# Performance work log

Measured on AMD Instinct MI355X. Metric: run time of the kernel, lower is better.

The kernel has to match this reference:

```python
import jax, jax.numpy as jnp
import numpy as np

LN_EPS = 1e-5


def layer_norm(x, g, b):
    m = jnp.mean(x, axis=-1, keepdims=True)
    v = jnp.mean(jnp.square(x - m), axis=-1, keepdims=True)
    return (x - m) * jax.lax.rsqrt(v + LN_EPS) * g + b


def sym_norm(A):
    # D^{-1/2} (A + I) D^{-1/2}
    N = A.shape[0]
    Ah = A + jnp.eye(N, dtype=A.dtype)
    d = jnp.sum(Ah, axis=-1)
    dinv = jax.lax.rsqrt(jnp.maximum(d, 1e-12))
    return Ah * dinv[:, None] * dinv[None, :]


def gru_layer(xs, Wih, Whh, bih, bhh):
    # xs: (BN, T, Din) -> ys: (BN, T, H). PyTorch GRU cell math.
    BN, T, _ = xs.shape
    H = Whh.shape[1]
    x_proj = xs @ Wih.T + bih  # (BN, T, 3H), precompute input projections

    def step(h, xp):
        hp = h @ Whh.T + bhh
        xr, xz, xn = jnp.split(xp, 3, axis=-1)
        hr, hz, hn = jnp.split(hp, 3, axis=-1)
        r = jax.nn.sigmoid(xr + hr)
        z = jax.nn.sigmoid(xz + hz)
        n = jnp.tanh(xn + r * hn)
        h_new = (1.0 - z) * n + z * h
        return h_new, h_new

    h0 = jnp.zeros((BN, H), xs.dtype)
    _, ys = jax.lax.scan(step, h0, jnp.swapaxes(x_proj, 0, 1))
    return jnp.swapaxes(ys, 0, 1)


def amscf_forward(x, A, FSP, DSP,
                  E1, E2, fus_W, fus_b, fus_v, beta1, beta2,
                  gcn_W1, gcn_b1, ln1_g, ln1_b, gcn_W2, gcn_b2, ln2_g, ln2_b,
                  gru_Wih0, gru_Whh0, gru_bih0, gru_bhh0,
                  gru_Wih1, gru_Whh1, gru_bih1, gru_bhh1,
                  att_w, fc1_W, fc1_b, fc2_W, fc2_b):
    B, T, N, _ = x.shape
    Hor = fc2_W.shape[0]

    # ImprovedAdjacency: blend A with adaptive node-embedding adjacency
    Aadp = jax.nn.softmax(jax.nn.relu(E1 @ E2.T), axis=-1)
    IA = 0.5 * A + 0.5 * Aadp

    # fuse_with_A with learned gates
    w1 = jax.nn.sigmoid(beta1)
    w2 = jax.nn.sigmoid(beta2)
    C1 = w1 * A + (1.0 - w1) * FSP
    C2 = w2 * A + (1.0 - w2) * DSP

    # TransposeAttentionFusion: graph-level attention over the 3 candidate graphs
    Gs = jnp.stack([IA, C1, C2], axis=0)  # (3, N, N)
    sc = jnp.mean(jnp.tanh(Gs @ fus_W.T + fus_b) @ fus_v, axis=-1)  # (3,)
    alpha = jax.nn.softmax(sc)
    MG = jnp.einsum('k,knm->nm', alpha, Gs)

    S_hat = sym_norm(MG)  # (N, N)

    # TwoLayerGCN over all (B, T) at once: act(LN(S X W1)) -> LN(S h W2)
    xf = x.reshape(B * T, N, 1)
    h = jnp.einsum('mn,bnc->bmc', S_hat, xf) @ gcn_W1 + gcn_b1
    h = jax.nn.relu(layer_norm(h, ln1_g, ln1_b))
    g = jnp.einsum('mn,bnc->bmc', S_hat, h) @ gcn_W2 + gcn_b2
    g = layer_norm(g, ln2_g, ln2_b)  # (B*T, N, C)

    C = g.shape[-1]
    # Faithful to original: raw view of (B, T, N, C) into (B*N, T, C)
    H_seq = g.reshape(B, T, N, C).reshape(B * N, T, C)

    out = gru_layer(H_seq, gru_Wih0, gru_Whh0, gru_bih0, gru_bhh0)
    out = gru_layer(out, gru_Wih1, gru_Whh1, gru_bih1, gru_bhh1)  # (BN, T, Hg)

    # SoftAttentionPooling over time
    score = out @ att_w  # (BN, T)
    att = jax.nn.softmax(score, axis=1)
    ctx = jnp.einsum('bt,bth->bh', att, out)

    hfc = jax.nn.gelu(ctx @ fc1_W.T + fc1_b)
    dlt = hfc @ fc2_W.T + fc2_b  # (BN, Hor); dropout is identity at eval
    return jnp.transpose(dlt.reshape(B, N, Hor), (0, 2, 1))  # (B, Hor, N)


def setup_inputs() -> dict:
    B, T, N, Hor = 32, 12, 1000, 12
    Cin, Ch, Cout, Hg, Da, De = 1, 96, 96, 192, 32, 10
    key = jax.random.key(0)
    ks = jax.random.split(key, 32)
    f32 = jnp.float32

    def nrm(k, shape, scale):
        return jax.random.normal(k, shape, dtype=f32) * scale

    inp = {
        'x': jax.random.normal(ks[0], (B, T, N, Cin), dtype=f32),
        'A': jax.random.uniform(ks[1], (N, N), dtype=f32),
        'FSP': jax.random.uniform(ks[2], (N, N), dtype=f32),
        'DSP': jax.random.uniform(ks[3], (N, N), dtype=f32),
        'E1': nrm(ks[4], (N, De), 0.1),
        'E2': nrm(ks[5], (N, De), 0.1),
        'fus_W': nrm(ks[6], (Da, N), 1.0 / np.sqrt(N)),
        'fus_b': jnp.zeros((Da,), f32),
        'fus_v': nrm(ks[7], (Da,), 1.0 / np.sqrt(Da)),
        'beta1': jnp.float32(0.5),
        'beta2': jnp.float32(0.5),
        'gcn_W1': nrm(ks[8], (Cin, Ch), 1.0 / np.sqrt(Cin)),
        'gcn_b1': jnp.zeros((Ch,), f32),
        'ln1_g': jnp.ones((Ch,), f32),
        'ln1_b': jnp.zeros((Ch,), f32),
        'gcn_W2': nrm(ks[9], (Ch, Cout), 1.0 / np.sqrt(Ch)),
        'gcn_b2': jnp.zeros((Cout,), f32),
        'ln2_g': jnp.ones((Cout,), f32),
        'ln2_b': jnp.zeros((Cout,), f32),
        'gru_Wih0': nrm(ks[10], (3 * Hg, Cout), 1.0 / np.sqrt(Hg)),
        'gru_Whh0': nrm(ks[11], (3 * Hg, Hg), 1.0 / np.sqrt(Hg)),
        'gru_bih0': jnp.zeros((3 * Hg,), f32),
        'gru_bhh0': jnp.zeros((3 * Hg,), f32),
        'gru_Wih1': nrm(ks[12], (3 * Hg, Hg), 1.0 / np.sqrt(Hg)),
        'gru_Whh1': nrm(ks[13], (3 * Hg, Hg), 1.0 / np.sqrt(Hg)),
        'gru_bih1': jnp.zeros((3 * Hg,), f32),
        'gru_bhh1': jnp.zeros((3 * Hg,), f32),
        'att_w': nrm(ks[14], (Hg,), 1.0 / np.sqrt(Hg)),
        'fc1_W': nrm(ks[15], (Hg, Hg), 1.0 / np.sqrt(Hg)),
        'fc1_b': jnp.zeros((Hg,), f32),
        'fc2_W': nrm(ks[16], (Hor, Hg), 1.0 / np.sqrt(Hg)),
        'fc2_b': jnp.zeros((Hor,), f32),
    }
    return inp


def reference(x, A, FSP, DSP, E1, E2, fus_W, fus_b, fus_v, beta1, beta2,
              gcn_W1, gcn_b1, ln1_g, ln1_b, gcn_W2, gcn_b2, ln2_g, ln2_b,
              gru_Wih0, gru_Whh0, gru_bih0, gru_bhh0,
              gru_Wih1, gru_Whh1, gru_bih1, gru_bhh1,
              att_w, fc1_W, fc1_b, fc2_W, fc2_b):
    return amscf_forward(x, A, FSP, DSP, E1, E2, fus_W, fus_b, fus_v, beta1, beta2,
                         gcn_W1, gcn_b1, ln1_g, ln1_b, gcn_W2, gcn_b2, ln2_g, ln2_b,
                         gru_Wih0, gru_Whh0, gru_bih0, gru_bhh0,
                         gru_Wih1, gru_Whh1, gru_bih1, gru_bhh1,
                         att_w, fc1_W, fc1_b, fc2_W, fc2_b)
```

## Files before the change

### kernel.cpp

```cpp
#include <hip/hip_runtime.h>

typedef unsigned short u16;
typedef unsigned int u32;
typedef __attribute__((ext_vector_type(8))) short short8;
typedef __attribute__((ext_vector_type(4))) float float4v;

#define DEV static __device__ __forceinline__

DEV float bf2f(u16 u) { u32 x = ((u32)u) << 16; float f; __builtin_memcpy(&f, &x, 4); return f; }
DEV u16 f2bf(float f) {
  u32 u; __builtin_memcpy(&u, &f, 4);
  u = (u + 0x7fffu + ((u >> 16) & 1u)) >> 16;
  return (u16)u;
}
DEV float sigm(float x) { return 1.f / (1.f + __expf(-x)); }

DEV void gl16(const u16* g, u16* l) {
  __builtin_amdgcn_global_load_lds(
      (const __attribute__((address_space(1))) void*)g,
      (__attribute__((address_space(3))) void*)l, 16, 0, 0);
}

template <int OMODE>
__launch_bounds__(256)
__global__ void gemm_nt(const u16* __restrict__ A, int lda,
                        const u16* __restrict__ B, int ldb,
                        void* __restrict__ Cp, int ldc,
                        int M, int N, int K,
                        const float* __restrict__ bias)
{
  constexpr int PK = 40;
  __shared__ u16 As[128 * PK];
  __shared__ u16 Bs[64 * PK];

  const int tid  = threadIdx.x;
  const int m0   = blockIdx.y * 128;
  const int n0   = blockIdx.x * 64;
  const int wid  = tid >> 6;
  const int lane = tid & 63;
  const int l15  = lane & 15;
  const int quad = lane >> 4;
  const int wm   = (wid >> 1) * 64;
  const int wn   = (wid & 1) * 32;

  float4v acc[4][2];
  const float4v fz = {0.f, 0.f, 0.f, 0.f};
#pragma unroll
  for (int i = 0; i < 4; i++)
#pragma unroll
    for (int j = 0; j < 2; j++) acc[i][j] = fz;

  const int arow = tid >> 2;
  const int akc  = tid & 3;

  const int kt_count = (K + 31) / 32;
  for (int kt = 0; kt < kt_count; ++kt) {
    const int k0 = kt * 32 + akc * 8;
    const bool kok = (k0 < K);
    uint4 av0 = make_uint4(0, 0, 0, 0), av1 = av0, bv = av0;
    int ra = m0 + arow;
    if (kok && ra < M)        av0 = *(const uint4*)(A + (size_t)ra * lda + k0);
    if (kok && ra + 64 < M)   av1 = *(const uint4*)(A + (size_t)(ra + 64) * lda + k0);
    int rb = n0 + arow;
    if (kok && rb < N)        bv  = *(const uint4*)(B + (size_t)rb * ldb + k0);

    __syncthreads();
    *(uint4*)&As[arow * PK + akc * 8]        = av0;
    *(uint4*)&As[(arow + 64) * PK + akc * 8] = av1;
    *(uint4*)&Bs[arow * PK + akc * 8]        = bv;
    __syncthreads();

    short8 af[4], bfr[2];
#pragma unroll
    for (int i = 0; i < 4; i++)
      af[i] = *(const short8*)&As[(wm + i * 16 + l15) * PK + quad * 8];
#pragma unroll
    for (int j = 0; j < 2; j++)
      bfr[j] = *(const short8*)&Bs[(wn + j * 16 + l15) * PK + quad * 8];
#pragma unroll
    for (int i = 0; i < 4; i++)
#pragma unroll
      for (int j = 0; j < 2; j++)
        acc[i][j] = __builtin_amdgcn_mfma_f32_16x16x32_bf16(af[i], bfr[j], acc[i][j], 0, 0, 0);
  }

#pragma unroll
  for (int i = 0; i < 4; i++)
#pragma unroll
    for (int j = 0; j < 2; j++)
#pragma unroll
      for (int e = 0; e < 4; e++) {
        int r = m0 + wm + i * 16 + quad * 4 + e;
        int c = n0 + wn + j * 16 + l15;
        if (r < M && c < N) {
          float v = acc[i][j][e];
          if (OMODE == 0) ((float*)Cp)[(size_t)r * ldc + c] = v;
          else {
            float a = v + bias[c];
            float t = tanhf(0.7978845608028654f * (a + 0.044715f * a * a * a));
            ((float*)Cp)[(size_t)r * ldc + c] = 0.5f * a * (1.f + t);
          }
        }
      }
}

__launch_bounds__(256)
__global__ void k_bigemm(const u16* __restrict__ A,
                         const u16* __restrict__ B,
                         const float* __restrict__ b2, const float* __restrict__ g2,
                         const float* __restrict__ be2,
                         u16* __restrict__ Gg)
{
  __shared__ u16 As[128 * 64];
  __shared__ u16 Bs[96 * 64];
  __shared__ float stats[2][2][128];

  const int tid  = threadIdx.x;
  const int bid  = blockIdx.x;
  const int xcd  = bid & 7;
  const int jj   = bid >> 3;
  const int m0   = (jj & 7) * 128;
  const int rt   = xcd + 8 * (jj >> 3);

  const int wid  = tid >> 6;
  const int lane = tid & 63;
  const int l15  = lane & 15;
  const int quad = lane >> 4;
  const int wm   = (wid >> 1) * 64;
  const int wn   = (wid & 1) * 48;
  const int wni  = wid & 1;

  const int srow8 = lane >> 3;
  const int sw8   = ((lane & 7) ^ srow8) * 8;

  const u16* abase = A + (size_t)(m0 + wid * 8 + srow8) * 1024 + sw8;
  const u16* bbase = B + (size_t)(rt * 96 + wid * 8 + srow8) * 1024 + sw8;

  float4v acc[4][3];
  const float4v fz = {0.f, 0.f, 0.f, 0.f};
#pragma unroll
  for (int i = 0; i < 4; i++)
#pragma unroll
    for (int j = 0; j < 3; j++) acc[i][j] = fz;

  for (int kt = 0; kt < 16; ++kt) {
    const int ko = kt * 64;
#pragma unroll
    for (int c = 0; c < 4; c++)
      gl16(abase + (size_t)c * 32 * 1024 + ko, &As[(c * 32 + wid * 8) * 64]);
#pragma unroll
    for (int c = 0; c < 3; c++)
      gl16(bbase + (size_t)c * 32 * 1024 + ko, &Bs[(c * 32 + wid * 8) * 64]);
    __syncthreads();
#pragma unroll
    for (int k32 = 0; k32 < 2; k32++) {
      const int swr = ((quad + 4 * k32) ^ (l15 & 7)) * 8;
      short8 af[4], bf[3];
#pragma unroll
      for (int i = 0; i < 4; i++)
        af[i] = *(const short8*)&As[(wm + i * 16 + l15) * 64 + swr];
#pragma unroll
      for (int j = 0; j < 3; j++)
        bf[j] = *(const short8*)&Bs[(wn + j * 16 + l15) * 64 + swr];
#pragma unroll
      for (int i = 0; i < 4; i++)
#pragma unroll
        for (int j = 0; j < 3; j++)
          acc[i][j] = __builtin_amdgcn_mfma_f32_16x16x32_bf16(af[i], bf[j], acc[i][j], 0, 0, 0);
    }
    __syncthreads();
  }

  float b2v[3], g2v[3], bev[3];
#pragma unroll
  for (int j = 0; j < 3; j++) {
    int c = wn + j * 16 + l15;
    b2v[j] = b2[c]; g2v[j] = g2[c]; bev[j] = be2[c];
  }
#pragma unroll
  for (int i = 0; i < 4; i++)
#pragma unroll
    for (int e = 0; e < 4; e++) {
      float s = 0.f, ss = 0.f;
#pragma unroll
      for (int j = 0; j < 3; j++) {
        float v = acc[i][j][e] + b2v[j];
        acc[i][j][e] = v;
        s += v; ss += v * v;
      }
      s += __shfl_xor(s, 1); ss += __shfl_xor(ss, 1);
      s += __shfl_xor(s, 2); ss += __shfl_xor(ss, 2);
      s += __shfl_xor(s, 4); ss += __shfl_xor(ss, 4);
      s += __shfl_xor(s, 8); ss += __shfl_xor(ss, 8);
      if (l15 == 0) {
        int rl = wm + i * 16 + quad * 4 + e;
        stats[wni][0][rl] = s;
        stats[wni][1][rl] = ss;
      }
    }
  __syncthreads();
#pragma unroll
  for (int i = 0; i < 4; i++)
#pragma unroll
    for (int e = 0; e < 4; e++) {
      int rl = wm + i * 16 + quad * 4 + e;
      int m = m0 + rl;
      if (m < 1000) {
        float ts  = stats[0][0][rl] + stats[1][0][rl];
        float tss = stats[0][1][rl] + stats[1][1][rl];
        float mean = ts * (1.f / 96.f);
        float var  = tss * (1.f / 96.f) - mean * mean;
        float isd  = rsqrtf(var + 1e-5f);
#pragma unroll
        for (int j = 0; j < 3; j++) {
          int c = wn + j * 16 + l15;
          Gg[(size_t)rt * 96000 + (size_t)m * 96 + c] =
              f2bf((acc[i][j][e] - mean) * isd * g2v[j] + bev[j]);
        }
      }
    }
}

DEV void pool_fold(int m0, int c0, int pm,
                   const u16* __restrict__ Hpool,
                   const float* __restrict__ score_rd,
                   const float* __restrict__ Mrd, const float* __restrict__ Lrd,
                   float* __restrict__ Mwr, float* __restrict__ Lwr,
                   float* __restrict__ Nvp)
{
  const int tid = threadIdx.x;
#pragma unroll
  for (int k = 0; k < 16; k++) {
    int idx = k * 256 + tid;
    int ql = idx >> 5, cl = idx & 31;
    int q = m0 + ql, c = c0 + cl;
    size_t nidx = (size_t)q * 192 + c;
    float s = score_rd[q];
    float hnew = bf2f(Hpool[nidx]);
    float so, wnf, prev;
    if (pm == 1) { so = 0.f; wnf = 1.f; prev = 0.f; }
    else {
      float Mo = Mrd[q];
      float Mn = fmaxf(Mo, s);
      so = __expf(Mo - Mn); wnf = __expf(s - Mn);
      prev = Nvp[nidx];
    }
    Nvp[nidx] = prev * so + wnf * hnew;
  }
  if (c0 == 0 && tid < 128) {
    int q = m0 + tid;
    float s = score_rd[q];
    if (pm == 1) { Mwr[q] = s; Lwr[q] = 1.f; }
    else {
      float Mo = Mrd[q], Mn = fmaxf(Mo, s);
      Mwr[q] = Mn;
      Lwr[q] = Lrd[q] * __expf(Mo - Mn) + __expf(s - Mn);
    }
  }
}

template <int KX, bool POOL>
DEV void gru_tile(u16* As, u16* Bs,
                  int m0, int c0,
                  const u16* __restrict__ Xin, int ldx,
                  const u16* __restrict__ Win,
                  const u16* __restrict__ Hin,
                  const u16* __restrict__ Whh,
                  const float* __restrict__ bih, const float* __restrict__ bhh,
                  u16* __restrict__ Hout,
                  const float* __restrict__ att_w,
                  float* __restrict__ score_acc,
                  const u16* __restrict__ Hpool,
                  const float* __restrict__ score_rd,
                  const float* __restrict__ Mrd, const float* __restrict__ Lrd,
                  float* __restrict__ Mwr, float* __restrict__ Lwr,
                  float* __restrict__ Nvp,
                  int t0, int pm)
{
  const int tid  = threadIdx.x;
  const int wid  = tid >> 6;
  const int lane = tid & 63;
  const int l15  = lane & 15;
  const int quad = lane >> 4;
  const int wm   = wid * 32;

  if (!POOL && pm)
    pool_fold(m0, c0, pm, Hpool, score_rd, Mrd, Lrd, Mwr, Lwr, Nvp);

  const int srow8 = lane >> 3;
  const int sw8   = ((lane & 7) ^ srow8) * 8;
  const int srow4 = lane >> 2;
  const int sw4   = ((lane & 3) ^ ((lane >> 3) & 3)) * 8;

  float4v aR[2][2], aZ[2][2], aXN[2][2], aHN[2][2];
  const float4v fz = {0.f, 0.f, 0.f, 0.f};
#pragma unroll
  for (int i = 0; i < 2; i++)
#pragma unroll
    for (int j = 0; j < 2; j++) { aR[i][j] = fz; aZ[i][j] = fz; aXN[i][j] = fz; aHN[i][j] = fz; }

  if (KX == 96) {
    const u16* ax0 = Xin + (size_t)(m0 + wid * 16 + srow4) * ldx + sw4;
    const u16* ax1 = Xin + (size_t)(m0 + 64 + wid * 16 + srow4) * ldx + sw4;
    const int b0 = wid * 16 + srow4;
    const u16* bx0 = Win + (size_t)((b0 >> 5) * 192 + c0 + (b0 & 31)) * 96 + sw4;
    const int b1 = 64 + wid * 16 + srow4;
    const u16* bx1 = Win + (size_t)(384 + c0 + (b1 & 31)) * 96 + sw4;
    u16* asl0 = &As[(wid * 16) * 32];
    u16* asl1 = &As[(64 + wid * 16) * 32];
    u16* bsl0 = &Bs[(wid * 16) * 32];
    u16* bsl1 = &Bs[(64 + wid * 16) * 32];
    const int swa = (quad ^ ((l15 >> 1) & 3)) * 8;
#pragma unroll
    for (int kt = 0; kt < 3; ++kt) {
      const int ko = kt * 32;
      gl16(ax0 + ko, asl0); gl16(ax1 + ko, asl1);
      gl16(bx0 + ko, bsl0);
      if (wid < 2) gl16(bx1 + ko, bsl1);
      __syncthreads();
      short8 af[2], bR[2], bZ[2], bN[2];
#pragma unroll
      for (int i = 0; i < 2; i++)
        af[i] = *(const short8*)&As[(wm + i * 16 + l15) * 32 + swa];
#pragma unroll
      for (int j = 0; j < 2; j++) {
        bR[j] = *(const short8*)&Bs[(j * 16 + l15) * 32 + swa];
        bZ[j] = *(const short8*)&Bs[(32 + j * 16 + l15) * 32 + swa];
        bN[j] = *(const short8*)&Bs[(64 + j * 16 + l15) * 32 + swa];
      }
#pragma unroll
      for (int i = 0; i < 2; i++)
#pragma unroll
        for (int j = 0; j < 2; j++) {
          aR[i][j]  = __builtin_amdgcn_mfma_f32_16x16x32_bf16(af[i], bR[j], aR[i][j], 0, 0, 0);
          aZ[i][j]  = __builtin_amdgcn_mfma_f32_16x16x32_bf16(af[i], bZ[j], aZ[i][j], 0, 0, 0);
          aXN[i][j] = __builtin_amdgcn_mfma_f32_16x16x32_bf16(af[i], bN[j], aXN[i][j], 0, 0, 0);
        }
      __syncthreads();
    }
  } else {
    const u16* abase = Xin + (size_t)(m0 + wid * 8 + srow8) * 192 + sw8;
    const u16* bbase = Win + (size_t)(c0 + wid * 8 + srow8) * 192 + sw8;
#pragma unroll
    for (int kt = 0; kt < 3; ++kt) {
      const int ko = kt * 64;
#pragma unroll
      for (int c = 0; c < 4; c++)
        gl16(abase + (size_t)c * 32 * 192 + ko, &As[(c * 32 + wid * 8) * 64]);
#pragma unroll
      for (int c = 0; c < 3; c++)
        gl16(bbase + (size_t)c * 192 * 192 + ko, &Bs[(c * 32 + wid * 8) * 64]);
      __syncthreads();
#pragma unroll
      for (int k32 = 0; k32 < 2; k32++) {
        const int swr = ((quad + 4 * k32) ^ (l15 & 7)) * 8;
        short8 af[2], bR[2], bZ[2], bN[2];
#pragma unroll
        for (int i = 0; i < 2; i++)
          af[i] = *(const short8*)&As[(wm + i * 16 + l15) * 64 + swr];
#pragma unroll
        for (int j = 0; j < 2; j++) {
          bR[j] = *(const short8*)&Bs[(j * 16 + l15) * 64 + swr];
          bZ[j] = *(const short8*)&Bs[(32 + j * 16 + l15) * 64 + swr];
          bN[j] = *(const short8*)&Bs[(64 + j * 16 + l15) * 64 + swr];
        }
#pragma unroll
        for (int i = 0; i < 2; i++)
#pragma unroll
          for (int j = 0; j < 2; j++) {
            aR[i][j]  = __builtin_amdgcn_mfma_f32_16x16x32_bf16(af[i], bR[j], aR[i][j], 0, 0, 0);
            aZ[i][j]  = __builtin_amdgcn_mfma_f32_16x16x32_bf16(af[i], bZ[j], aZ[i][j], 0, 0, 0);
            aXN[i][j] = __builtin_amdgcn_mfma_f32_16x16x32_bf16(af[i], bN[j], aXN[i][j], 0, 0, 0);
          }
      }
      __syncthreads();
    }
  }
  if (!t0) {
    const u16* abase = Hin + (size_t)(m0 + wid * 8 + srow8) * 192 + sw8;
    const u16* bbase = Whh + (size_t)(c0 + wid * 8 + srow8) * 192 + sw8;
#pragma unroll
    for (int kt = 0; kt < 3; ++kt) {
      const int ko = kt * 64;
#pragma unroll
      for (int c = 0; c < 4; c++)
        gl16(abase + (size_t)c * 32 * 192 + ko, &As[(c * 32 + wid * 8) * 64]);
#pragma unroll
      for (int c = 0; c < 3; c++)
        gl16(bbase + (size_t)c * 192 * 192 + ko, &Bs[(c * 32 + wid * 8) * 64]);
      __syncthreads();
#pragma unroll
      for (int k32 = 0; k32 < 2; k32++) {
        const int swr = ((quad + 4 * k32) ^ (l15 & 7)) * 8;
        short8 af[2], bR[2], bZ[2], bN[2];
#pragma unroll
        for (int i = 0; i < 2; i++)
          af[i] = *(const short8*)&As[(wm + i * 16 + l15) * 64 + swr];
#pragma unroll
        for (int j = 0; j < 2; j++) {
          bR[j] = *(const short8*)&Bs[(j * 16 + l15) * 64 + swr];
          bZ[j] = *(const short8*)&Bs[(32 + j * 16 + l15) * 64 + swr];
          bN[j] = *(const short8*)&Bs[(64 + j * 16 + l15) * 64 + swr];
        }
#pragma unroll
        for (int i = 0; i < 2; i++)
#pragma unroll
          for (int j = 0; j < 2; j++) {
            aR[i][j]  = __builtin_amdgcn_mfma_f32_16x16x32_bf16(af[i], bR[j], aR[i][j], 0, 0, 0);
            aZ[i][j]  = __builtin_amdgcn_mfma_f32_16x16x32_bf16(af[i], bZ[j], aZ[i][j], 0, 0, 0);
            aHN[i][j] = __builtin_amdgcn_mfma_f32_16x16x32_bf16(af[i], bN[j], aHN[i][j], 0, 0, 0);
          }
      }
      __syncthreads();
    }
  }

  float ps[2][4];
  if (POOL) {
#pragma unroll
    for (int i = 0; i < 2; i++)
#pragma unroll
      for (int e = 0; e < 4; e++) ps[i][e] = 0.f;
  }
#pragma unroll
  for (int j = 0; j < 2; ++j) {
    const int c = c0 + j * 16 + l15;
    const float brz = bih[c] + bhh[c];
    const float bzz = bih[192 + c] + bhh[192 + c];
    const float bxn = bih[384 + c];
    const float bhn = bhh[384 + c];
    const float aw  = POOL ? att_w[c] : 0.f;
#pragma unroll
    for (int i = 0; i < 2; ++i)
#pragma unroll
      for (int e = 0; e < 4; ++e) {
        const int row = m0 + wm + i * 16 + quad * 4 + e;
        float rg  = sigm(aR[i][j][e] + brz);
        float zg  = sigm(aZ[i][j][e] + bzz);
        float hnv = bhn + (t0 ? 0.f : aHN[i][j][e]);
        float ng  = tanhf(aXN[i][j][e] + bxn + rg * hnv);
        float hold = t0 ? 0.f : bf2f(Hin[(size_t)row * 192 + c]);
        float hnew = (1.f - zg) * ng + zg * hold;
        Hout[(size_t)row * 192 + c] = f2bf(hnew);
        if (POOL) ps[i][e] += hnew * aw;
      }
  }
  if (POOL) {
#pragma unroll
    for (int i = 0; i < 2; ++i)
#pragma unroll
      for (int e = 0; e < 4; ++e) {
        float v = ps[i][e];
        v += __shfl_xor(v, 1); v += __shfl_xor(v, 2);
        v += __shfl_xor(v, 4); v += __shfl_xor(v, 8);
        if (l15 == 0) atomicAdd(&score_acc[m0 + wm + i * 16 + quad * 4 + e], v);
      }
  }
}

struct GruArgs {
  const u16 *Gg, *Wih0, *Whh0, *Wih1, *Whh1;
  const float *bih0, *bhh0, *bih1, *bhh1, *att_w;
  u16 *h0[2];
  u16 *h1[3];
  float *M[2], *L[2], *s[3];
  float* Nv;
};

__launch_bounds__(256)
__global__ void k_gru2(GruArgs a, int u)
{
  __shared__ u16 As[128 * 64];
  __shared__ u16 Bs[96 * 64];
  const int m0 = blockIdx.y * 128;

  if (blockIdx.x < 6) {
    const int c0 = blockIdx.x * 32;
    const int pm = (u < 2) ? 0 : (u == 2 ? 1 : 2);
    if (u > 11) {
      if (pm)
        pool_fold(m0, c0, pm, a.h1[(u + 1) % 3], a.s[(u + 1) % 3],
                  a.M[(u + 1) & 1], a.L[(u + 1) & 1], a.M[u & 1], a.L[u & 1], a.Nv);
      return;
    }
    if (c0 == 0 && threadIdx.x < 128) a.s[u % 3][m0 + threadIdx.x] = 0.f;
    gru_tile<96, false>(As, Bs, m0, c0,
        a.Gg + u * 96, 1152, a.Wih0, a.h0[u & 1], a.Whh0, a.bih0, a.bhh0, a.h0[(u & 1) ^ 1],
        nullptr, nullptr,
        a.h1[(u + 1) % 3], a.s[(u + 1) % 3],
        a.M[(u + 1) & 1], a.L[(u + 1) & 1],
        a.M[u & 1], a.L[u & 1],
        a.Nv, u == 0, pm);
  } else {
    if (u < 1) return;
    const int t = u - 1;
    const int c0 = (blockIdx.x - 6) * 32;
    gru_tile<192, true>(As, Bs, m0, c0,
        a.h0[u & 1], 192, a.Wih1, a.h1[(u + 1) % 3], a.Whh1, a.bih1, a.bhh1, a.h1[t % 3],
        a.att_w, a.s[t % 3],
        nullptr, nullptr, nullptr, nullptr, nullptr, nullptr, nullptr,
        t == 0, 0);
  }
}

__launch_bounds__(256)
__global__ void k_pool(const u16* __restrict__ H, const float* __restrict__ score_rd,
                       const float* __restrict__ Mrd, const float* __restrict__ Lrd,
                       float* __restrict__ Lwr, float* __restrict__ Nv)
{
  const int base = blockIdx.x * 1536;
  const int tid  = threadIdx.x;
#pragma unroll
  for (int k = 0; k < 6; k++) {
    const int idx = base + tid + k * 256;
    const int q = idx / 192;
    const float s = score_rd[q];
    const float Mo = Mrd[q];
    const float Mn = fmaxf(Mo, s);
    const float so = __expf(Mo - Mn);
    const float wn = __expf(s - Mn);
    Nv[idx] = Nv[idx] * so + wn * bf2f(H[idx]);
  }
  if (tid < 8) {
    const int q = blockIdx.x * 8 + tid;
    const float s = score_rd[q];
    const float Mo = Mrd[q];
    const float Mn = fmaxf(Mo, s);
    Lwr[q] = Lrd[q] * __expf(Mo - Mn) + __expf(s - Mn);
  }
}

__launch_bounds__(256)
__global__ void k_h2gemm(const float* __restrict__ yt, const float4* __restrict__ cwpk,
                         const u16* __restrict__ W2s, const float* __restrict__ consts,
                         u16* __restrict__ h2t)
{
  constexpr int PK = 40;
  __shared__ u16 As[128 * PK];
  __shared__ u16 Bs[96 * PK];
  __shared__ u16 Ts[96 * 136];

  const int tid  = threadIdx.x;
  const int m0   = blockIdx.x * 128;
  const int wid  = tid >> 6;
  const int lane = tid & 63;
  const int l15  = lane & 15;
  const int quad = lane >> 4;
  const int wm   = (wid >> 1) * 64;
  const int wn   = (wid & 1) * 48;

  const float P = consts[0], Q = consts[1], VW = consts[2], CWB = consts[3], VB = consts[4];

  const int arow = tid >> 2;
  const int akc  = tid & 3;

  float yv[2], mu[2], iv[2];
#pragma unroll
  for (int rr = 0; rr < 2; rr++) {
    int i = m0 + arow + rr * 64;
    int r = i / 1000, n = i - r * 1000;
    float y = yt[n * 384 + r];
    yv[rr] = y;
    mu[rr] = y * P + Q;
    iv[rr] = rsqrtf(y * y * VW + 2.f * y * CWB + VB + 1e-5f);
  }

  float4v acc[4][3];
  const float4v fz = {0.f, 0.f, 0.f, 0.f};
#pragma unroll
  for (int i = 0; i < 4; i++)
#pragma unroll
    for (int j = 0; j < 3; j++) acc[i][j] = fz;

  uint4 asave[2][3];
  const bool has2 = (arow < 32);

  for (int kt = 0; kt < 6; ++kt) {
    const int k0 = kt * 32 + akc * 8;
    uint4 av[2];
    if (kt < 3) {
#pragma unroll
      for (int rr = 0; rr < 2; rr++) {
        u16 hb[8];
#pragma unroll
        for (int e = 0; e < 8; e++) {
          float4 cw = cwpk[k0 + e];
          float t = yv[rr] * cw.x + cw.y - mu[rr];
          float h = fmaxf(t * iv[rr] * cw.z + cw.w, 0.f);
          hb[e] = f2bf(h);
        }
        __builtin_memcpy(&av[rr], hb, 16);
        asave[rr][kt] = av[rr];
      }
    } else {
      av[0] = asave[0][kt - 3];
      av[1] = asave[1][kt - 3];
    }
    uint4 bv0 = *(const uint4*)(W2s + (size_t)arow * 192 + k0);
    uint4 bv1 = make_uint4(0, 0, 0, 0);
    if (has2) bv1 = *(const uint4*)(W2s + (size_t)(arow + 64) * 192 + k0);

    __syncthreads();
    *(uint4*)&As[arow * PK + akc * 8]        = av[0];
    *(uint4*)&As[(arow + 64) * PK + akc * 8] = av[1];
    *(uint4*)&Bs[arow * PK + akc * 8]        = bv0;
    if (has2) *(uint4*)&Bs[(arow + 64) * PK + akc * 8] = bv1;
    __syncthreads();

    short8 af[4], bfr[3];
#pragma unroll
    for (int i = 0; i < 4; i++)
      af[i] = *(const short8*)&As[(wm + i * 16 + l15) * PK + quad * 8];
#pragma unroll
    for (int j = 0; j < 3; j++)
      bfr[j] = *(const short8*)&Bs[(wn + j * 16 + l15) * PK + quad * 8];
#pragma unroll
    for (int i = 0; i < 4; i++)
#pragma unroll
      for (int j = 0; j < 3; j++)
        acc[i][j] = __builtin_amdgcn_mfma_f32_16x16x32_bf16(af[i], bfr[j], acc[i][j], 0, 0, 0);
  }

#pragma unroll
  for (int i = 0; i < 4; i++)
#pragma unroll
    for (int j = 0; j < 3; j++)
#pragma unroll
      for (int e = 0; e < 4; e++) {
        int rowl = wm + i * 16 + quad * 4 + e;
        int c2   = wn + j * 16 + l15;
        Ts[c2 * 136 + rowl] = f2bf(acc[i][j][e]);
      }
  __syncthreads();
#pragma unroll
  for (int u = tid; u < 1536; u += 256) {
    int c2 = u >> 4, ch = u & 15;
    int iidx0 = m0 + ch * 8;
    int r = iidx0 / 1000, n0 = iidx0 - r * 1000;
    *(uint4*)(h2t + (size_t)(r * 96 + c2) * 1024 + n0) = *(const uint4*)&Ts[c2 * 136 + ch * 8];
  }
}

__launch_bounds__(256)
__global__ void k_prep(const float* x, const float* fus_W,
                       const float* Wih0, const float* Whh0,
                       const float* Wih1, const float* Whh1,
                       const float* gcn_W1, const float* gcn_b1,
                       const float* gcn_W2, const float* ln1g, const float* ln1b,
                       u16* xbf, u16* fusWbf, u16* Wih0b, u16* Whh0b, u16* Wih1b, u16* Whh1b,
                       u16* W2s, float4* cwpk, float* consts)
{
  long o = (long)blockIdx.x * 256 + threadIdx.x;
  if (o < 384000) xbf[o] = f2bf(x[o]);
  else if ((o -= 384000) < 32000) fusWbf[o] = f2bf(fus_W[o]);
  else if ((o -= 32000) < 55296)  Wih0b[o] = f2bf(Wih0[o]);
  else if ((o -= 55296) < 110592) Whh0b[o] = f2bf(Whh0[o]);
  else if ((o -= 110592) < 110592) Wih1b[o] = f2bf(Wih1[o]);
  else if ((o -= 110592) < 110592) Whh1b[o] = f2bf(Whh1[o]);
  else if ((o -= 110592) < 9216) {
    int c2 = (int)o / 96, c = (int)o - c2 * 96;
    float wv = gcn_W2[c * 96 + c2];
    u16 hi = f2bf(wv);
    u16 lo = f2bf(wv - bf2f(hi));
    W2s[c2 * 192 + c] = hi;
    W2s[c2 * 192 + 96 + c] = lo;
  }
  else if ((o -= 9216) < 96) {
    int c = (int)o;
    float4 cw;
    cw.x = gcn_W1[c]; cw.y = gcn_b1[c]; cw.z = ln1g[c]; cw.w = ln1b[c];
    cwpk[c] = cw;
  }
  if (blockIdx.x == 0 && threadIdx.x == 0) {
    float sw = 0, sb = 0, sww = 0, swb = 0, sbb = 0;
    for (int c = 0; c < 96; c++) {
      float wv = gcn_W1[c], b = gcn_b1[c];
      sw += wv; sb += b; sww += wv * wv; swb += wv * b; sbb += b * b;
    }
    float P = sw / 96.f, Q = sb / 96.f;
    consts[0] = P; consts[1] = Q;
    consts[2] = sww / 96.f - P * P;
    consts[3] = swb / 96.f - P * Q;
    consts[4] = sbb / 96.f - Q * Q;
  }
}

__launch_bounds__(256)
__global__ void k_zero(u16* __restrict__ h2t, float* __restrict__ s0,
                       float* __restrict__ s1, float* __restrict__ s2)
{
  int idx = blockIdx.x * 256 + threadIdx.x;
  if (idx < 110592) {
    int row = idx / 3, p = idx - row * 3;
    *(uint4*)(h2t + (size_t)row * 1024 + 1000 + p * 8) = make_uint4(0, 0, 0, 0);
  } else if ((idx -= 110592) < 32000) {
    s0[idx] = 0.f;
  } else if ((idx -= 32000) < 32000) {
    s1[idx] = 0.f;
  } else if ((idx -= 32000) < 32000) {
    s2[idx] = 0.f;
  }
}

__launch_bounds__(256)
__global__ void k_w1split(const float* __restrict__ fc1W, u16* __restrict__ w1s)
{
  int idx = blockIdx.x * 256 + threadIdx.x;
  if (idx >= 192 * 192) return;
  int n = idx / 192, k = idx - n * 192;
  float w = fc1W[idx];
  u16 hi = f2bf(w);
  u16 lo = f2bf(w - bf2f(hi));
  w1s[(size_t)n * 576 + k]       = hi;
  w1s[(size_t)n * 576 + 192 + k] = lo;
  w1s[(size_t)n * 576 + 384 + k] = hi;
}

__launch_bounds__(256)
__global__ void k_adjrow(const float* __restrict__ A, const float* __restrict__ FSP,
                         const float* __restrict__ DSP, const float* __restrict__ E1,
                         const float* __restrict__ E2,
                         const float* beta1, const float* beta2,
                         u16* __restrict__ G, float* __restrict__ rowsums)
{
  __shared__ float z[1000];
  __shared__ float red[256];
  const int n = blockIdx.x, tid = threadIdx.x;

  float e1r[10];
#pragma unroll
  for (int d = 0; d < 10; d++) e1r[d] = E1[n * 10 + d];

  float lmax = -1e30f;
  for (int m = tid; m < 1000; m += 256) {
    float s = 0;
#pragma unroll
    for (int d = 0; d < 10; d++) s += e1r[d] * E2[m * 10 + d];
    s = fmaxf(s, 0.f);
    z[m] = s;
    lmax = fmaxf(lmax, s);
  }
  red[tid] = lmax; __syncthreads();
  for (int st = 128; st > 0; st >>= 1) { if (tid < st) red[tid] = fmaxf(red[tid], red[tid + st]); __syncthreads(); }
  const float mx = red[0]; __syncthreads();

  float lsum = 0;
  for (int m = tid; m < 1000; m += 256) { float e = __expf(z[m] - mx); z[m] = e; lsum += e; }
  red[tid] = lsum; __syncthreads();
  for (int st = 128; st > 0; st >>= 1) { if (tid < st) red[tid] += red[tid + st]; __syncthreads(); }
  const float inv = 1.f / red[0]; __syncthreads();

  const float w1 = sigm(beta1[0]);
  const float w2 = sigm(beta2[0]);
  float s0 = 0, s1 = 0, s2 = 0;
  for (int m = tid; m < 1000; m += 256) {
    float aadp = z[m] * inv;
    float a = A[n * 1000 + m], f = FSP[n * 1000 + m], dd = DSP[n * 1000 + m];
    float g0 = 0.5f * a + 0.5f * aadp;
    float g1 = w1 * a + (1.f - w1) * f;
    float g2 = w2 * a + (1.f - w2) * dd;
    G[0 * 1000000 + n * 1000 + m] = f2bf(g0);
    G[1 * 1000000 + n * 1000 + m] = f2bf(g1);
    G[2 * 1000000 + n * 1000 + m] = f2bf(g2);
    s0 += g0; s1 += g1; s2 += g2;
  }
  red[tid] = s0; __syncthreads();
  for (int st = 128; st > 0; st >>= 1) { if (tid < st) red[tid] += red[tid + st]; __syncthreads(); }
  if (tid == 0) rowsums[n] = red[0];
  __syncthreads();
  red[tid] = s1; __syncthreads();
  for (int st = 128; st > 0; st >>= 1) { if (tid < st) red[tid] += red[tid + st]; __syncthreads(); }
  if (tid == 0) rowsums[1000 + n] = red[0];
  __syncthreads();
  red[tid] = s2; __syncthreads();
  for (int st = 128; st > 0; st >>= 1) { if (tid < st) red[tid] += red[tid + st]; __syncthreads(); }
  if (tid == 0) rowsums[2000 + n] = red[0];
}

__launch_bounds__(256)
__global__ void k_sc(const float* __restrict__ P, const float* fus_b, const float* fus_v, float* sc)
{
  __shared__ float red[256];
  const int k = blockIdx.x, tid = threadIdx.x;
  float local = 0;
  for (int n = tid; n < 1000; n += 256) {
    const float* p = P + (size_t)(k * 1000 + n) * 32;
    float s = 0;
#pragma unroll
    for (int a = 0; a < 32; a++) s += tanhf(p[a] + fus_b[a]) * fus_v[a];
    local += s;
  }
  red[tid] = local; __syncthreads();
  for (int st = 128; st > 0; st >>= 1) { if (tid < st) red[tid] += red[tid + st]; __syncthreads(); }
  if (tid == 0) sc[k] = red[0] * (1.f / 1000.f);
}

__launch_bounds__(256)
__global__ void k_alpha(const float* sc, const float* rowsums, float* alpha_out, float* dinv)
{
  __shared__ float al[3];
  const int tid = threadIdx.x;
  if (tid == 0) {
    float m = fmaxf(sc[0], fmaxf(sc[1], sc[2]));
    float e0 = __expf(sc[0] - m), e1 = __expf(sc[1] - m), e2 = __expf(sc[2] - m);
    float inv = 1.f / (e0 + e1 + e2);
    al[0] = e0 * inv; al[1] = e1 * inv; al[2] = e2 * inv;
    alpha_out[0] = al[0]; alpha_out[1] = al[1]; alpha_out[2] = al[2];
  }
  __syncthreads();
  const float a0 = al[0], a1 = al[1], a2 = al[2];
  for (int n = tid; n < 1000; n += 256) {
    float d = a0 * rowsums[n] + a1 * rowsums[1000 + n] + a2 * rowsums[2000 + n] + 1.0f;
    dinv[n] = rsqrtf(fmaxf(d, 1e-12f));
  }
}

__launch_bounds__(256)
__global__ void k_shat(const u16* __restrict__ G, const float* alpha, const float* dinv,
                       u16* __restrict__ S)
{
  int idx = blockIdx.x * 256 + threadIdx.x;
  if (idx >= 1024000) return;
  int i = idx >> 10, j = idx & 1023;
  u16 val = 0;
  if (j < 1000) {
    const float a0 = alpha[0], a1 = alpha[1], a2 = alpha[2];
    int g = i * 1000 + j;
    float mg = a0 * bf2f(G[g]) + a1 * bf2f(G[1000000 + g]) + a2 * bf2f(G[2000000 + g]);
    if (i == j) mg += 1.0f;
    val = f2bf(mg * dinv[i] * dinv[j]);
  }
  S[(size_t)i * 1024 + j] = val;
}

__launch_bounds__(256)
__global__ void k_ctxsplit(const float* __restrict__ Nv, const float* __restrict__ Lbuf,
                           u16* __restrict__ ctxs)
{
  const int i = blockIdx.x * 256 + threadIdx.x;
  if (i >= 32000 * 192) return;
  const int q = i / 192, c = i - q * 192;
  float v = Nv[i] / Lbuf[q];
  u16 hi = f2bf(v);
  u16 lo = f2bf(v - bf2f(hi));
  u16* row = ctxs + (size_t)q * 576;
  row[c] = hi; row[192 + c] = hi; row[384 + c] = lo;
}

__launch_bounds__(192)
__global__ void k_fc2(const float* __restrict__ hfc, const float* __restrict__ fc2W,
                      const float* __restrict__ fc2b, float* __restrict__ out)
{
  __shared__ float w2S[12][193];
  __shared__ float hS[16][193];
  const int tid = threadIdx.x;
  const int q0 = blockIdx.x * 16;
  for (int idx = tid; idx < 12 * 192; idx += 192) {
    int o = idx / 192, k = idx - o * 192;
    w2S[o][k] = fc2W[idx];
  }
  for (int idx = tid; idx < 16 * 192; idx += 192) {
    int qq = idx / 192, k = idx - qq * 192;
    hS[qq][k] = hfc[(size_t)(q0 + qq) * 192 + k];
  }
  __syncthreads();
  const int qq = tid / 12, o = tid - qq * 12;
  float acc = fc2b[o];
#pragma unroll 8
  for (int k = 0; k < 192; k++) acc += hS[qq][k] * w2S[o][k];
  const int q = q0 + qq;
  const int b = q / 1000, node = q - b * 1000;
  out[(size_t)b * 12000 + o * 1000 + node] = acc;
}

extern "C" void kernel_launch(void* const* d_in, const int* in_sizes, int n_in,
                              void* d_out, int out_size, void* d_ws, size_t ws_size,
                              hipStream_t stream)
{
  const float* x     = (const float*)d_in[0];
  const float* A     = (const float*)d_in[1];
  const float* FSP   = (const float*)d_in[2];
  const float* DSP   = (const float*)d_in[3];
  const float* E1    = (const float*)d_in[4];
  const float* E2    = (const float*)d_in[5];
  const float* fus_W = (const float*)d_in[6];
  const float* fus_b = (const float*)d_in[7];
  const float* fus_v = (const float*)d_in[8];
  const float* beta1 = (const float*)d_in[9];
  const float* beta2 = (const float*)d_in[10];
  const float* gcn_W1= (const float*)d_in[11];
  const float* gcn_b1= (const float*)d_in[12];
  const float* ln1g  = (const float*)d_in[13];
  const float* ln1b  = (const float*)d_in[14];
  const float* gcn_W2= (const float*)d_in[15];
  const float* gcn_b2= (const float*)d_in[16];
  const float* ln2g  = (const float*)d_in[17];
  const float* ln2b  = (const float*)d_in[18];
  const float* Wih0  = (const float*)d_in[19];
  const float* Whh0  = (const float*)d_in[20];
  const float* bih0  = (const float*)d_in[21];
  const float* bhh0  = (const float*)d_in[22];
  const float* Wih1  = (const float*)d_in[23];
  const float* Whh1  = (const float*)d_in[24];
  const float* bih1  = (const float*)d_in[25];
  const float* bhh1  = (const float*)d_in[26];
  const float* att_w = (const float*)d_in[27];
  const float* fc1W  = (const float*)d_in[28];
  const float* fc1b  = (const float*)d_in[29];
  const float* fc2W  = (const float*)d_in[30];
  const float* fc2b  = (const float*)d_in[31];
  float* out = (float*)d_out;

  char* w = (char*)d_ws;
  auto alloc = [&](size_t bytes) -> char* {
    char* p = w;
    w += (bytes + 255) & ~(size_t)255;
    return p;
  };

  float* consts  = (float*)alloc(8 * 4);
  float* scp     = (float*)alloc(3 * 4);
  float* alphap  = (float*)alloc(3 * 4);
  float* rowsums = (float*)alloc(3000 * 4);
  float* dinvp   = (float*)alloc(1000 * 4);
  u16*   Gbuf    = (u16*)alloc((size_t)3000000 * 2);
  u16*   Sbf     = (u16*)alloc((size_t)1024 * 1024 * 2);
  u16*   xbf     = (u16*)alloc((size_t)384000 * 2);
  u16*   fusWbf  = (u16*)alloc((size_t)32000 * 2);
  u16*   Wih0b   = (u16*)alloc((size_t)55296 * 2);
  u16*   Whh0b   = (u16*)alloc((size_t)110592 * 2);
  u16*   Wih1b   = (u16*)alloc((size_t)110592 * 2);
  u16*   Whh1b   = (u16*)alloc((size_t)110592 * 2);
  u16*   w1s     = (u16*)alloc((size_t)192 * 576 * 2);
  u16*   W2s     = (u16*)alloc((size_t)96 * 192 * 2);
  float4* cwpk   = (float4*)alloc((size_t)96 * 16);
  float* Pbuf    = (float*)alloc((size_t)96000 * 4);
  float* yt      = (float*)alloc((size_t)384000 * 4);
  u16*   h2t     = (u16*)alloc((size_t)36864 * 1024 * 2);
  u16*   Gg      = (u16*)alloc((size_t)36864000 * 2);
  float* Nv      = (float*)alloc((size_t)6144000 * 4);
  float* Mb0     = (float*)alloc((size_t)32000 * 4);
  float* Mb1     = (float*)alloc((size_t)32000 * 4);
  float* Lb0     = (float*)alloc((size_t)32000 * 4);
  float* Lb1     = (float*)alloc((size_t)32000 * 4);
  float* sc0     = (float*)alloc((size_t)32000 * 4);
  float* sc1     = (float*)alloc((size_t)32000 * 4);
  float* sc2     = (float*)alloc((size_t)32000 * 4);

  u16* h0s[2] = { h2t,                    h2t + (size_t)6144000 };
  u16* h1s[3] = { h2t + (size_t)12288000, h2t + (size_t)18432000, h2t + (size_t)24576000 };
  u16*   ctxs = h2t;
  float* hfc  = (float*)(h2t + (size_t)18432000);

  k_prep<<<3174, 256, 0, stream>>>(x, fus_W, Wih0, Whh0, Wih1, Whh1, gcn_W1, gcn_b1,
                                   gcn_W2, ln1g, ln1b,
                                   xbf, fusWbf, Wih0b, Whh0b, Wih1b, Whh1b, W2s, cwpk, consts);
  k_w1split<<<144, 256, 0, stream>>>(fc1W, w1s);
  k_zero<<<807, 256, 0, stream>>>(h2t, sc0, sc1, sc2);
  k_adjrow<<<1000, 256, 0, stream>>>(A, FSP, DSP, E1, E2, beta1, beta2, Gbuf, rowsums);
  gemm_nt<0><<<dim3(1, 24), 256, 0, stream>>>(Gbuf, 1000, fusWbf, 1000, Pbuf, 32, 3000, 32, 1000, nullptr);
  k_sc<<<3, 256, 0, stream>>>(Pbuf, fus_b, fus_v, scp);
  k_alpha<<<1, 256, 0, stream>>>(scp, rowsums, alphap, dinvp);
  k_shat<<<4000, 256, 0, stream>>>(Gbuf, alphap, dinvp, Sbf);
  gemm_nt<0><<<dim3(6, 8), 256, 0, stream>>>(Sbf, 1024, xbf, 1000, yt, 384, 1000, 384, 1000, nullptr);
  k_h2gemm<<<3000, 256, 0, stream>>>(yt, cwpk, W2s, consts, h2t);
  k_bigemm<<<3072, 256, 0, stream>>>(Sbf, h2t, gcn_b2, ln2g, ln2b, Gg);

  GruArgs ga;
  ga.Gg = Gg; ga.Wih0 = Wih0b; ga.Whh0 = Whh0b; ga.Wih1 = Wih1b; ga.Whh1 = Whh1b;
  ga.bih0 = bih0; ga.bhh0 = bhh0; ga.bih1 = bih1; ga.bhh1 = bhh1; ga.att_w = att_w;
  ga.h0[0] = h0s[0]; ga.h0[1] = h0s[1];
  ga.h1[0] = h1s[0]; ga.h1[1] = h1s[1]; ga.h1[2] = h1s[2];
  ga.M[0] = Mb0; ga.M[1] = Mb1; ga.L[0] = Lb0; ga.L[1] = Lb1;
  ga.s[0] = sc0; ga.s[1] = sc1; ga.s[2] = sc2;
  ga.Nv = Nv;
  for (int u = 0; u <= 12; ++u)
    k_gru2<<<dim3(12, 250), 256, 0, stream>>>(ga, u);

  k_pool<<<4000, 256, 0, stream>>>(h1s[2], sc2, Mb0, Lb0, Lb1, Nv);

  k_ctxsplit<<<24000, 256, 0, stream>>>(Nv, Lb1, ctxs);
  gemm_nt<3><<<dim3(3, 250), 256, 0, stream>>>(ctxs, 576, w1s, 576, hfc, 192, 32000, 192, 576, fc1b);
  k_fc2<<<2000, 192, 0, stream>>>(hfc, fc2W, fc2b, out);
}
```

Measured before the change: 1.448 ms.

## Fuse prep/zero/w1split kernels, fold fusion-score GEMM into adjrow, merge pool into ctxsplit

Merges the weight-split and zeroing kernels into k_prep and folds the per-graph attention-score GEMM plus tanh reduction into k_adjrow. k_adjrow keeps its row in shared memory, projects it against a transposed fus_W, and atomically accumulates the scores. The final online-softmax pooling step is folded into k_ctxsplit, which removes a separate pass over the 6M-element Nv buffer. Together these cut kernel launches and global round trips. The cost is heavier k_adjrow blocks with more shared memory, and float atomics that make the score sum order nondeterministic.

```diff
diff --git a/kernel.cpp b/kernel.cpp
--- a/kernel.cpp
+++ b/kernel.cpp
@@ -504,33 +504,6 @@
 }
 
 __launch_bounds__(256)
-__global__ void k_pool(const u16* __restrict__ H, const float* __restrict__ score_rd,
-                       const float* __restrict__ Mrd, const float* __restrict__ Lrd,
-                       float* __restrict__ Lwr, float* __restrict__ Nv)
-{
-  const int base = blockIdx.x * 1536;
-  const int tid  = threadIdx.x;
-#pragma unroll
-  for (int k = 0; k < 6; k++) {
-    const int idx = base + tid + k * 256;
-    const int q = idx / 192;
-    const float s = score_rd[q];
-    const float Mo = Mrd[q];
-    const float Mn = fmaxf(Mo, s);
-    const float so = __expf(Mo - Mn);
-    const float wn = __expf(s - Mn);
-    Nv[idx] = Nv[idx] * so + wn * bf2f(H[idx]);
-  }
-  if (tid < 8) {
-    const int q = blockIdx.x * 8 + tid;
-    const float s = score_rd[q];
-    const float Mo = Mrd[q];
-    const float Mn = fmaxf(Mo, s);
-    Lwr[q] = Lrd[q] * __expf(Mo - Mn) + __expf(s - Mn);
-  }
-}
-
-__launch_bounds__(256)
 __global__ void k_h2gemm(const float* __restrict__ yt, const float4* __restrict__ cwpk,
                          const u16* __restrict__ W2s, const float* __restrict__ consts,
                          u16* __restrict__ h2t)
@@ -647,8 +620,10 @@
                        const float* Wih1, const float* Whh1,
                        const float* gcn_W1, const float* gcn_b1,
                        const float* gcn_W2, const float* ln1g, const float* ln1b,
+                       const float* fc1W,
                        u16* xbf, u16* fusWbf, u16* Wih0b, u16* Whh0b, u16* Wih1b, u16* Whh1b,
-                       u16* W2s, float4* cwpk, float* consts)
+                       u16* W2s, float4* cwpk, float* scp, u16* w1s, float* fusWT,
+                       u16* h2t, float* s0, float* s1, float* s2, float* consts)
 {
   long o = (long)blockIdx.x * 256 + threadIdx.x;
   if (o < 384000) xbf[o] = f2bf(x[o]);
@@ -671,6 +646,29 @@
     cw.x = gcn_W1[c]; cw.y = gcn_b1[c]; cw.z = ln1g[c]; cw.w = ln1b[c];
     cwpk[c] = cw;
   }
+  else if ((o -= 96) < 3) scp[o] = 0.f;
+  else if ((o -= 3) < 36864) {
+    int n = (int)o / 192, k = (int)o - n * 192;
+    float wv = fc1W[o];
+    u16 hi = f2bf(wv);
+    u16 lo = f2bf(wv - bf2f(hi));
+    w1s[(size_t)n * 576 + k]       = hi;
+    w1s[(size_t)n * 576 + 192 + k] = lo;
+    w1s[(size_t)n * 576 + 384 + k] = hi;
+  }
+  else if ((o -= 36864) < 32000) {
+    int m = (int)o >> 5, a = (int)o & 31;
+    fusWT[o] = fus_W[a * 1000 + m];
+  }
+  else if ((o -= 32000) < 110592) {
+    int row = (int)o / 3, p = (int)o - row * 3;
+    *(uint4*)(h2t + (size_t)row * 1024 + 1000 + p * 8) = make_uint4(0, 0, 0, 0);
+  }
+  else if ((o -= 110592) < 96000) {
+    if (o < 32000) s0[o] = 0.f;
+    else if (o < 64000) s1[o - 32000] = 0.f;
+    else s2[o - 64000] = 0.f;
+  }
   if (blockIdx.x == 0 && threadIdx.x == 0) {
     float sw = 0, sb = 0, sww = 0, swb = 0, sbb = 0;
     for (int c = 0; c < 96; c++) {
@@ -686,45 +684,20 @@
 }
 
 __launch_bounds__(256)
-__global__ void k_zero(u16* __restrict__ h2t, float* __restrict__ s0,
-                       float* __restrict__ s1, float* __restrict__ s2)
-{
-  int idx = blockIdx.x * 256 + threadIdx.x;
-  if (idx < 110592) {
-    int row = idx / 3, p = idx - row * 3;
-    *(uint4*)(h2t + (size_t)row * 1024 + 1000 + p * 8) = make_uint4(0, 0, 0, 0);
-  } else if ((idx -= 110592) < 32000) {
-    s0[idx] = 0.f;
-  } else if ((idx -= 32000) < 32000) {
-    s1[idx] = 0.f;
-  } else if ((idx -= 32000) < 32000) {
-    s2[idx] = 0.f;
-  }
-}
-
-__launch_bounds__(256)
-__global__ void k_w1split(const float* __restrict__ fc1W, u16* __restrict__ w1s)
-{
-  int idx = blockIdx.x * 256 + threadIdx.x;
-  if (idx >= 192 * 192) return;
-  int n = idx / 192, k = idx - n * 192;
-  float w = fc1W[idx];
-  u16 hi = f2bf(w);
-  u16 lo = f2bf(w - bf2f(hi));
-  w1s[(size_t)n * 576 + k]       = hi;
-  w1s[(size_t)n * 576 + 192 + k] = lo;
-  w1s[(size_t)n * 576 + 384 + k] = hi;
-}
-
-__launch_bounds__(256)
 __global__ void k_adjrow(const float* __restrict__ A, const float* __restrict__ FSP,
                          const float* __restrict__ DSP, const float* __restrict__ E1,
                          const float* __restrict__ E2,
                          const float* beta1, const float* beta2,
-                         u16* __restrict__ G, float* __restrict__ rowsums)
+                         const float* __restrict__ fusWT,
+                         const float* __restrict__ fus_b, const float* __restrict__ fus_v,
+                         u16* __restrict__ G, float* __restrict__ rowsums,
+                         float* __restrict__ scp)
 {
   __shared__ float z[1000];
   __shared__ float red[256];
+  __shared__ float gk[3000];
+  __shared__ float pred[768];
+  __shared__ float vred[96];
   const int n = blockIdx.x, tid = threadIdx.x;
 
   float e1r[10];
@@ -762,6 +735,7 @@
     G[0 * 1000000 + n * 1000 + m] = f2bf(g0);
     G[1 * 1000000 + n * 1000 + m] = f2bf(g1);
     G[2 * 1000000 + n * 1000 + m] = f2bf(g2);
+    gk[m] = g0; gk[1000 + m] = g1; gk[2000 + m] = g2;
     s0 += g0; s1 += g1; s2 += g2;
   }
   red[tid] = s0; __syncthreads();
@@ -775,24 +749,34 @@
   red[tid] = s2; __syncthreads();
   for (int st = 128; st > 0; st >>= 1) { if (tid < st) red[tid] += red[tid + st]; __syncthreads(); }
   if (tid == 0) rowsums[2000 + n] = red[0];
-}
-
-__launch_bounds__(256)
-__global__ void k_sc(const float* __restrict__ P, const float* fus_b, const float* fus_v, float* sc)
-{
-  __shared__ float red[256];
-  const int k = blockIdx.x, tid = threadIdx.x;
-  float local = 0;
-  for (int n = tid; n < 1000; n += 256) {
-    const float* p = P + (size_t)(k * 1000 + n) * 32;
-    float s = 0;
-#pragma unroll
-    for (int a = 0; a < 32; a++) s += tanhf(p[a] + fus_b[a]) * fus_v[a];
-    local += s;
-  }
-  red[tid] = local; __syncthreads();
-  for (int st = 128; st > 0; st >>= 1) { if (tid < st) red[tid] += red[tid + st]; __syncthreads(); }
-  if (tid == 0) sc[k] = red[0] * (1.f / 1000.f);
+  __syncthreads();
+
+  const int a = tid & 31, grp = tid >> 5;
+  float p0 = 0.f, p1 = 0.f, p2 = 0.f;
+  for (int m = grp; m < 1000; m += 8) {
+    float wv = fusWT[m * 32 + a];
+    p0 += gk[m] * wv;
+    p1 += gk[1000 + m] * wv;
+    p2 += gk[2000 + m] * wv;
+  }
+  pred[0 * 256 + a * 8 + grp] = p0;
+  pred[1 * 256 + a * 8 + grp] = p1;
+  pred[2 * 256 + a * 8 + grp] = p2;
+  __syncthreads();
+  if (tid < 96) {
+    int k = tid >> 5, aa = tid & 31;
+    float P = 0.f;
+#pragma unroll
+    for (int g = 0; g < 8; g++) P += pred[k * 256 + aa * 8 + g];
+    vred[k * 32 + aa] = tanhf(P + fus_b[aa]) * fus_v[aa];
+  }
+  __syncthreads();
+  if (tid < 3) {
+    float s = 0.f;
+#pragma unroll
+    for (int aa = 0; aa < 32; aa++) s += vred[tid * 32 + aa];
+    atomicAdd(&scp[tid], s * 0.001f);
+  }
 }
 
 __launch_bounds__(256)
@@ -834,13 +818,21 @@
 }
 
 __launch_bounds__(256)
-__global__ void k_ctxsplit(const float* __restrict__ Nv, const float* __restrict__ Lbuf,
+__global__ void k_ctxsplit(const float* __restrict__ Nv, const u16* __restrict__ Hlast,
+                           const float* __restrict__ score_rd,
+                           const float* __restrict__ Mrd, const float* __restrict__ Lrd,
                            u16* __restrict__ ctxs)
 {
   const int i = blockIdx.x * 256 + threadIdx.x;
   if (i >= 32000 * 192) return;
   const int q = i / 192, c = i - q * 192;
-  float v = Nv[i] / Lbuf[q];
+  const float s = score_rd[q];
+  const float Mo = Mrd[q];
+  const float Mn = fmaxf(Mo, s);
+  const float so = __expf(Mo - Mn);
+  const float wn = __expf(s - Mn);
+  const float L = Lrd[q] * so + wn;
+  float v = (Nv[i] * so + wn * bf2f(Hlast[i])) / L;
   u16 hi = f2bf(v);
   u16 lo = f2bf(v - bf2f(hi));
   u16* row = ctxs + (size_t)q * 576;
@@ -934,7 +926,7 @@
   u16*   w1s     = (u16*)alloc((size_t)192 * 576 * 2);
   u16*   W2s     = (u16*)alloc((size_t)96 * 192 * 2);
   float4* cwpk   = (float4*)alloc((size_t)96 * 16);
-  float* Pbuf    = (float*)alloc((size_t)96000 * 4);
+  float* fusWT   = (float*)alloc((size_t)32000 * 4);
   float* yt      = (float*)alloc((size_t)384000 * 4);
   u16*   h2t     = (u16*)alloc((size_t)36864 * 1024 * 2);
   u16*   Gg      = (u16*)alloc((size_t)36864000 * 2);
@@ -952,14 +944,12 @@
   u16*   ctxs = h2t;
   float* hfc  = (float*)(h2t + (size_t)18432000);
 
-  k_prep<<<3174, 256, 0, stream>>>(x, fus_W, Wih0, Whh0, Wih1, Whh1, gcn_W1, gcn_b1,
-                                   gcn_W2, ln1g, ln1b,
-                                   xbf, fusWbf, Wih0b, Whh0b, Wih1b, Whh1b, W2s, cwpk, consts);
-  k_w1split<<<144, 256, 0, stream>>>(fc1W, w1s);
-  k_zero<<<807, 256, 0, stream>>>(h2t, sc0, sc1, sc2);
-  k_adjrow<<<1000, 256, 0, stream>>>(A, FSP, DSP, E1, E2, beta1, beta2, Gbuf, rowsums);
-  gemm_nt<0><<<dim3(1, 24), 256, 0, stream>>>(Gbuf, 1000, fusWbf, 1000, Pbuf, 32, 3000, 32, 1000, nullptr);
-  k_sc<<<3, 256, 0, stream>>>(Pbuf, fus_b, fus_v, scp);
+  k_prep<<<4250, 256, 0, stream>>>(x, fus_W, Wih0, Whh0, Wih1, Whh1, gcn_W1, gcn_b1,
+                                   gcn_W2, ln1g, ln1b, fc1W,
+                                   xbf, fusWbf, Wih0b, Whh0b, Wih1b, Whh1b, W2s, cwpk,
+                                   scp, w1s, fusWT, h2t, sc0, sc1, sc2, consts);
+  k_adjrow<<<1000, 256, 0, stream>>>(A, FSP, DSP, E1, E2, beta1, beta2,
+                                     fusWT, fus_b, fus_v, Gbuf, rowsums, scp);
   k_alpha<<<1, 256, 0, stream>>>(scp, rowsums, alphap, dinvp);
   k_shat<<<4000, 256, 0, stream>>>(Gbuf, alphap, dinvp, Sbf);
   gemm_nt<0><<<dim3(6, 8), 256, 0, stream>>>(Sbf, 1024, xbf, 1000, yt, 384, 1000, 384, 1000, nullptr);
@@ -977,9 +967,7 @@
   for (int u = 0; u <= 12; ++u)
     k_gru2<<<dim3(12, 250), 256, 0, stream>>>(ga, u);
 
-  k_pool<<<4000, 256, 0, stream>>>(h1s[2], sc2, Mb0, Lb0, Lb1, Nv);
-
-  k_ctxsplit<<<24000, 256, 0, stream>>>(Nv, Lb1, ctxs);
+  k_ctxsplit<<<24000, 256, 0, stream>>>(Nv, h1s[2], sc2, Mb0, Lb0, ctxs);
   gemm_nt<3><<<dim3(3, 250), 256, 0, stream>>>(ctxs, 576, w1s, 576, hfc, 192, 32000, 192, 576, fc1b);
   k_fc2<<<2000, 192, 0, stream>>>(hfc, fc2W, fc2b, out);
 }
```

After: 1.425 ms. Within noise of the previous version (-1.6%).
